# Optimization experiments

Measured on AMD Instinct MI355X. Metric: run time of the kernel, lower is better.

The kernel has to match this reference:

```python
import jax, jax.numpy as jnp
import numpy as np
from jax import lax

V = 5001   # vocab_size = len(word2id)+1
E = 128    # embedding_dim
H = 256    # hidden_dim
HH = H // 2  # per-direction hidden
T = 9      # tag_len
B, S = 256, 512


def setup_inputs() -> dict:
    key = jax.random.key(0)
    ks = jax.random.split(key, 16)
    sc = 0.08
    n = lambda k, shp: (jax.random.normal(k, shp) * sc).astype(jnp.float32)
    return {
        "x": jax.random.randint(ks[0], (B, S), 0, V),
        "mask": jnp.ones((B, S), jnp.float32),
        "embed_table": n(ks[1], (V, E)),
        "Wih_f": n(ks[2], (4 * HH, E)), "Whh_f": n(ks[3], (4 * HH, HH)),
        "bih_f": n(ks[4], (4 * HH,)), "bhh_f": n(ks[5], (4 * HH,)),
        "Wih_b": n(ks[6], (4 * HH, E)), "Whh_b": n(ks[7], (4 * HH, HH)),
        "bih_b": n(ks[8], (4 * HH,)), "bhh_b": n(ks[9], (4 * HH,)),
        "W_out": n(ks[10], (T, H)), "b_out": n(ks[11], (T,)),
        "transitions": n(ks[12], (T, T)),
        "start_trans": n(ks[13], (T,)),
        "end_trans": n(ks[14], (T,)),
    }


def _lstm_dir(xs, Wih, Whh, bih, bhh, reverse):
    # xs: [S,B,E]; torch gate order i,f,g,o
    Bx = xs.shape[1]
    h0 = jnp.zeros((Bx, HH), xs.dtype)
    pre_x = jnp.einsum('sbe,ge->sbg', xs, Wih) + bih + bhh  # hoist input proj

    def step(carry, px):
        h, c = carry
        g = px + h @ Whh.T
        i, f, gg, o = jnp.split(g, 4, axis=-1)
        c = jax.nn.sigmoid(f) * c + jax.nn.sigmoid(i) * jnp.tanh(gg)
        h = jax.nn.sigmoid(o) * jnp.tanh(c)
        return (h, c), h

    _, hs = lax.scan(step, (h0, h0), pre_x, reverse=reverse)
    return hs  # [S,B,HH]


def _viterbi(emissions, mask, transitions, start_trans, end_trans):
    # emissions: [B,S,T], mask: [B,S] bool -> tags [B,S] int32, best score [B]
    Bx = emissions.shape[0]
    em_t = emissions.transpose(1, 0, 2)        # [S,B,T]
    score0 = start_trans + em_t[0]             # [B,T]
    idT = jnp.arange(T, dtype=jnp.int32)

    def step(score, inp):
        em, m = inp                            # em [B,T], m [B]
        cand = score[:, :, None] + transitions[None]     # [B,Tprev,Tcur]
        best = jnp.max(cand, axis=1) + em
        bp = jnp.argmax(cand, axis=1).astype(jnp.int32)  # [B,T]
        new_score = jnp.where(m[:, None], best, score)
        bp = jnp.where(m[:, None], bp, idT[None, :])
        return new_score, bp

    score, bps = lax.scan(step, score0, (em_t[1:], mask.T[1:]))  # bps [S-1,B,T]
    score = score + end_trans
    best_score = jnp.max(score, axis=-1)                          # [B]
    last = jnp.argmax(score, axis=-1).astype(jnp.int32)           # [B]

    def back(tag, bp_t):
        prev = jnp.take_along_axis(bp_t, tag[:, None], axis=1)[:, 0]
        return prev, prev

    _, prevs = lax.scan(back, last, bps, reverse=True)            # [S-1,B]
    tags = jnp.concatenate([prevs, last[None, :]], axis=0).T      # [B,S]
    return tags, best_score


def reference(x, mask, embed_table, Wih_f, Whh_f, bih_f, bhh_f,
              Wih_b, Whh_b, bih_b, bhh_b, W_out, b_out,
              transitions, start_trans, end_trans):
    emb = embed_table[x]                       # [B,S,E]
    xs = emb.transpose(1, 0, 2)                # [S,B,E]
    hf = _lstm_dir(xs, Wih_f, Whh_f, bih_f, bhh_f, reverse=False)
    hb = _lstm_dir(xs, Wih_b, Whh_b, bih_b, bhh_b, reverse=True)
    hs = jnp.concatenate([hf, hb], axis=-1).transpose(1, 0, 2)   # [B,S,H]
    # dropout is identity at inference
    em = hs @ W_out.T + b_out                  # [B,S,T]
    em = em * mask[..., None]
    tags, best_score = _viterbi(em, mask > 0, transitions, start_trans, end_trans)
    return tags, best_score
```

## Files before the change

### kernel.cpp

```cpp
#include <hip/hip_runtime.h>
#include <hip/hip_bf16.h>
#include <math.h>

#define S_LEN 512
#define B_SZ  256
#define E_DIM 128
#define HHID  128
#define G4    512
#define T_TAG 9
#define NR    (S_LEN * B_SZ)
#define VOCAB 5001
#define VOCABP 5008

typedef __attribute__((ext_vector_type(8))) short bf16x8;
typedef __attribute__((ext_vector_type(4))) float f32x4;

__device__ __forceinline__ float bf2f(__hip_bfloat16 v) { return __bfloat162float(v); }
__device__ __forceinline__ float scrub0(float v) {
    unsigned u = __float_as_uint(v);
    return (((u >> 23) & 0xFFu) == 0xFFu) ? 0.f : v;
}
__device__ __forceinline__ float frcp(float x) { return __builtin_amdgcn_rcpf(x); }
__device__ __forceinline__ float fsig(float x) { return frcp(1.f + __expf(-x)); }
__device__ __forceinline__ float ftanh(float x) {
    return 1.f - 2.f * frcp(1.f + __expf(2.f * x));
}

__device__ __hip_bfloat16 g_emb[VOCAB * E_DIM];
__device__ __hip_bfloat16 g_wih[2][G4 * E_DIM];
__device__ __hip_bfloat16 g_whh2[2][G4 * HHID];
__device__ __align__(16) float g_bias[2][G4];
__device__ float g_wout[T_TAG * 256];
__device__ float g_bout[T_TAG];
__device__ float g_trans[T_TAG * T_TAG];
__device__ float g_start[T_TAG];
__device__ float g_end[T_TAG];
__device__ float g_maskf[B_SZ * S_LEN];
__device__ float g_em[(long)NR * T_TAG];
__device__ __align__(16) float g_hs[2][(long)NR * HHID];
__device__ __align__(16) float g_pxv[(long)2 * VOCABP * 128 * 4];

__global__ __launch_bounds__(256) void convert_kernel(
    const void* mask, const void* emb,
    const void* wih_f, const void* whh_f, const void* bih_f, const void* bhh_f,
    const void* wih_b, const void* whh_b, const void* bih_b, const void* bhh_b,
    const void* wout, const void* bout, const void* trans,
    const void* startt, const void* endt, float* out, int out_size)
{
    const bool isb = (((const unsigned*)mask)[0] == 0x3F803F80u);
    auto ldf = [&](const void* p, long i) -> float {
        float v = isb ? bf2f(((const __hip_bfloat16*)p)[i]) : ((const float*)p)[i];
        return scrub0(v);
    };
    const long tid0   = (long)blockIdx.x * blockDim.x + threadIdx.x;
    const long stride = (long)gridDim.x * blockDim.x;

    for (long i = tid0; i < out_size; i += stride) out[i] = 0.f;
    for (long i = tid0; i < (long)VOCAB * E_DIM; i += stride)
        g_emb[i] = __float2bfloat16(ldf(emb, i));
    for (long i = tid0; i < (long)G4 * E_DIM; i += stride) {
        const int np = (int)(i >> 7), e = (int)(i & 127);
        const int g = np & 3, u = np >> 2;
        const long src = (long)(g * 128 + u) * E_DIM + e;
        g_wih[0][i] = __float2bfloat16(ldf(wih_f, src));
        g_wih[1][i] = __float2bfloat16(ldf(wih_b, src));
    }
    for (long i = tid0; i < (long)G4 * HHID; i += stride) {
        const int np = (int)(i >> 7), k = (int)(i & 127);
        const int g = np & 3, u = np >> 2;
        const long src = (long)(g * 128 + u) * HHID + k;
        g_whh2[0][i] = __float2bfloat16(ldf(whh_f, src));
        g_whh2[1][i] = __float2bfloat16(ldf(whh_b, src));
    }
    for (long i = tid0; i < G4; i += stride) {
        const int g = (int)i & 3, u = (int)i >> 2;
        const long src = g * 128 + u;
        g_bias[0][i] = ldf(bih_f, src) + ldf(bhh_f, src);
        g_bias[1][i] = ldf(bih_b, src) + ldf(bhh_b, src);
    }
    for (long i = tid0; i < T_TAG * 256; i += stride) g_wout[i] = ldf(wout, i);
    for (long i = tid0; i < T_TAG * T_TAG; i += stride) g_trans[i] = ldf(trans, i);
    for (long i = tid0; i < T_TAG; i += stride) {
        g_bout[i]  = ldf(bout, i);
        g_start[i] = ldf(startt, i);
        g_end[i]   = ldf(endt, i);
    }
    for (long i = tid0; i < (long)B_SZ * S_LEN; i += stride)
        g_maskf[i] = ldf(mask, i);
}

__global__ __launch_bounds__(512, 2) void pxv_gemm()
{
    const int grp = blockIdx.x, dir = blockIdx.y;
    const int tid  = threadIdx.x;
    const int lane = tid & 63, wv = tid >> 6;
    const int m16  = lane & 15, quad = lane >> 4;

    bf16x8 V[4][4];
    f32x4 bias4[4];
    #pragma unroll
    for (int t = 0; t < 4; t++) {
        const int np = (wv * 4 + t) * 16 + m16;
        #pragma unroll
        for (int kk = 0; kk < 4; kk++)
            V[t][kk] = *(const bf16x8*)&g_wih[dir][(long)np * E_DIM + kk * 32 + quad * 8];
        const int u = 16 * wv + 4 * t + quad;
        const float4 b4 = *(const float4*)&g_bias[dir][4 * u];
        bias4[t] = (f32x4){b4.x, b4.y, b4.z, b4.w};
    }
    const int v  = grp * 16 + m16;
    const int vv = (v < VOCAB) ? v : 0;
    bf16x8 E[4];
    #pragma unroll
    for (int kk = 0; kk < 4; kk++)
        E[kk] = *(const bf16x8*)&g_emb[(long)vv * E_DIM + kk * 32 + quad * 8];
    #pragma unroll
    for (int t = 0; t < 4; t++) {
        f32x4 px = bias4[t];
        #pragma unroll
        for (int kk = 0; kk < 4; kk++)
            px = __builtin_amdgcn_mfma_f32_16x16x32_bf16(V[t][kk], E[kk], px, 0, 0, 0);
        const int u = 16 * wv + 4 * t + quad;
        if (v < VOCAB)
            *(f32x4*)&g_pxv[((long)(dir * VOCABP + v) * 128 + u) * 4] = px;
    }
}

#define SCAN_STEP(RD, PX)                                                      \
  {                                                                            \
    const int wr_ = (RD) ^ 1;                                                  \
        \
    int se2_ = sev + 2 * step;                                                 \
    se2_ = se2_ < 0 ? 0 : (se2_ > S_LEN - 1 ? S_LEN - 1 : se2_);               \
    const float* pf_ = pxvL + xO[se2_ * 16 + m16];                             \
    bf16x8 Hh_[4], Hl_[4];                                                     \
    _Pragma("unroll")                                                          \
    for (int kk = 0; kk < 4; kk++) {                                           \
        const int off_ = ((kk * 4 + quad) * 16 + m16) * 8;                     \
        Hh_[kk] = *(const bf16x8*)&hB[RD][0][off_];                            \
        Hl_[kk] = *(const bf16x8*)&hB[RD][1][off_];                            \
    }                                                                          \
    _Pragma("unroll")                                                          \
    for (int t = 0; t < 4; t++) {                                              \
        _Pragma("unroll")                                                      \
        for (int kk = 0; kk < 4; kk++) {                                       \
            PX[t] = __builtin_amdgcn_mfma_f32_16x16x32_bf16(W[t][kk], Hh_[kk], PX[t], 0, 0, 0); \
            PX[t] = __builtin_amdgcn_mfma_f32_16x16x32_bf16(W[t][kk], Hl_[kk], PX[t], 0, 0, 0); \
        }                                                                      \
    }                                                                          \
    _Pragma("unroll")                                                          \
    for (int t = 0; t < 4; t++) {                                              \
        const float iv = fsig(PX[t][0]);                                       \
        const float fv = fsig(PX[t][1]);                                       \
        const float gv = ftanh(PX[t][2]);                                      \
        const float ov = fsig(PX[t][3]);                                       \
        c[t] = fv * c[t] + iv * gv;                                            \
        const float h = ov * ftanh(c[t]);                                      \
        const int u = 16 * wv + 4 * t + quad;                                  \
        const unsigned ub = __float_as_uint(h);                                \
        const unsigned hb_ = ub >> 16;                                         \
        const float hif = __uint_as_float(ub & 0xFFFF0000u);                   \
        const unsigned lb_ = __float_as_uint(h - hif) >> 16;                   \
        const int ha = (u >> 3) * 128 + m16 * 8 + (u & 7);                     \
        hB[wr_][0][ha] = (unsigned short)hb_;                                  \
        hB[wr_][1][ha] = (unsigned short)lb_;                                  \
        hsp[t * 64] = h;                                                       \
    }                                                                          \
    {          \
        PX[0] = *(const f32x4*)(pf_ + 0);                                      \
        PX[1] = *(const f32x4*)(pf_ + 16);                                     \
        PX[2] = *(const f32x4*)(pf_ + 32);                                     \
        PX[3] = *(const f32x4*)(pf_ + 48);                                     \
    }                                                                          \
    asm volatile("s_waitcnt lgkmcnt(0)" ::: "memory");                         \
    __builtin_amdgcn_sched_barrier(0);                                         \
    __builtin_amdgcn_s_barrier();                                              \
    __builtin_amdgcn_sched_barrier(0);                                         \
    hsp += hsd; sev += step; itv++;                                            \
  }

__global__ __launch_bounds__(512, 2) void scan_mfma(const int* __restrict__ x)
{
    __shared__ __align__(16) unsigned short hB[2][2][16 * 16 * 8];
    __shared__ int xO[S_LEN * 16];

    const int bg = blockIdx.x, dir = blockIdx.y;
    const int tid  = threadIdx.x;
    const int lane = tid & 63, wv = tid >> 6;
    const int m16  = lane & 15, quad = lane >> 4;

    bf16x8 W[4][4];
    #pragma unroll
    for (int t = 0; t < 4; t++) {
        const int np = (wv * 4 + t) * 16 + m16;
        #pragma unroll
        for (int kk = 0; kk < 4; kk++)
            W[t][kk] = *(const bf16x8*)&g_whh2[dir][(long)np * HHID + kk * 32 + quad * 8];
    }
    {
        const bool x64 = ((x[1] | x[3] | x[5] | x[7]) == 0);
        for (int i = tid; i < S_LEN * 16; i += 512) {
            const int s = i >> 4, m = i & 15;
            const int ii = (bg * 16 + m) * S_LEN + s;
            int tok = x64 ? x[2 * ii] : x[ii];
            tok = (unsigned)tok < VOCAB ? tok : 0;
            xO[i] = tok * 512;
        }
    }
    for (int i = tid; i < 2 * 2 * 2048; i += 512) ((unsigned short*)hB)[i] = 0;
    float c[4] = {0.f, 0.f, 0.f, 0.f};
    __syncthreads();

    const int se0  = dir ? (S_LEN - 1) : 0;
    const int step = dir ? -1 : 1;
    const int u0   = 16 * wv + quad;

    const float* pxvL = &g_pxv[(long)dir * VOCABP * 512 + u0 * 4];

    f32x4 pxA[4], pxB[4];
    {
        const int o0 = xO[se0 * 16 + m16];
        #pragma unroll
        for (int t = 0; t < 4; t++) pxA[t] = *(const f32x4*)(pxvL + o0 + 16 * t);
        const int se1 = (S_LEN > 1) ? se0 + step : se0;
        const int o1 = xO[se1 * 16 + m16];
        #pragma unroll
        for (int t = 0; t < 4; t++) pxB[t] = *(const f32x4*)(pxvL + o1 + 16 * t);
    }

    float* hsp = &g_hs[dir][((long)(se0 * 16 + bg) * 128 + u0) * 16 + m16];
    const long hsd = (long)step * 32768;

    int itv = 0, sev = se0;

    for (int it = 0; it < S_LEN; it += 2) {
        SCAN_STEP(0, pxA)
        SCAN_STEP(1, pxB)
    }
}

__global__ __launch_bounds__(256, 4) void emission_kernel()
{
    __shared__ float hfL[2048], hbL[2048];
    __shared__ float Wsh[T_TAG][256];
    __shared__ float bo[T_TAG];
    const int tid = threadIdx.x, blk = blockIdx.x;
    for (int i = tid; i < T_TAG * 256; i += 256) Wsh[i >> 8][i & 255] = g_wout[i];
    if (tid < T_TAG) bo[tid] = g_bout[tid];
    const float* hf = &g_hs[0][(long)blk * 2048];
    const float* hb = &g_hs[1][(long)blk * 2048];
    for (int i = tid; i < 2048; i += 256) { hfL[i] = hf[i]; hbL[i] = hb[i]; }
    __syncthreads();

    const int m = tid & 15, j = tid >> 4;
    if (j < T_TAG) {
        float acc = bo[j];
        #pragma unroll 4
        for (int u = 0; u < 128; u++)
            acc += hfL[u * 16 + m] * Wsh[j][u] + hbL[u * 16 + m] * Wsh[j][128 + u];
        const int r = (blk >> 4) * 256 + (blk & 15) * 16 + m;
        g_em[(long)r * T_TAG + j] = scrub0(acc);
    }
}

__global__ __launch_bounds__(256, 2)
void viterbi_kernel(float* __restrict__ out, int out_size)
{
    __shared__ unsigned char bp[4][S_LEN][T_TAG];
    const int wid  = threadIdx.x >> 6;
    const int lane = threadIdx.x & 63;
    const int b  = blockIdx.x * 4 + wid;
    const int jj = (lane < T_TAG) ? lane : 0;

    float tcol[T_TAG];
    #pragma unroll
    for (int i = 0; i < T_TAG; i++) tcol[i] = g_trans[i * T_TAG + jj];

    float score[T_TAG];
    {
        const float m0 = g_maskf[b * S_LEN + 0];
        #pragma unroll
        for (int i = 0; i < T_TAG; i++)
            score[i] = g_start[i] + g_em[(long)b * T_TAG + i] * m0;
    }
    float e = g_em[((long)1 * B_SZ + b) * T_TAG + jj];
    float m = g_maskf[b * S_LEN + 1];

    for (int s = 1; s < S_LEN; s++) {
        float en = 0.f, mn = 0.f;
        if (s + 1 < S_LEN) {
            en = g_em[((long)(s + 1) * B_SZ + b) * T_TAG + jj];
            mn = g_maskf[b * S_LEN + s + 1];
        }
        float best = score[0] + tcol[0];
        int arg = 0;
        #pragma unroll
        for (int i = 1; i < T_TAG; i++) {
            const float cnd = score[i] + tcol[i];
            if (cnd > best) { best = cnd; arg = i; }
        }
        float ns; int nbp;
        if (m > 0.f) { ns = best + e * m; nbp = arg; }
        else         { ns = score[jj];    nbp = jj;  }
        if (lane < T_TAG) bp[wid][s][jj] = (unsigned char)nbp;
        #pragma unroll
        for (int i = 0; i < T_TAG; i++) score[i] = __shfl(ns, i, 64);
        e = en; m = mn;
    }
    #pragma unroll
    for (int i = 0; i < T_TAG; i++) score[i] += g_end[i];

    __syncthreads();

    if (lane == 0) {
        float bs = score[0]; int last = 0;
        #pragma unroll
        for (int i = 1; i < T_TAG; i++)
            if (score[i] > bs) { bs = score[i]; last = i; }
        {
            const unsigned u = __float_as_uint(bs);
            if (((u >> 23) & 0xFFu) == 0xFFu) bs = -100.f;
        }
        if ((long)B_SZ * S_LEN + b < out_size)
            out[(long)B_SZ * S_LEN + b] = bs;
        int tag = last;
        if (tag < 0) tag = 0; if (tag > 8) tag = 8;
        out[(long)b * S_LEN + (S_LEN - 1)] = (float)tag;
        for (int s2 = S_LEN - 1; s2 >= 1; s2--) {
            tag = bp[wid][s2][tag];
            if (tag < 0) tag = 0; if (tag > 8) tag = 8;
            out[(long)b * S_LEN + (s2 - 1)] = (float)tag;
        }
    }
}

extern "C" void kernel_launch(void* const* d_in, const int* in_sizes, int n_in,
                              void* d_out, int out_size, void* d_ws, size_t ws_size,
                              hipStream_t stream) {
    const int* x = (const int*)d_in[0];
    float* out = (float*)d_out;

    convert_kernel<<<512, 256, 0, stream>>>(
        d_in[1], d_in[2], d_in[3], d_in[4], d_in[5], d_in[6],
        d_in[7], d_in[8], d_in[9], d_in[10], d_in[11], d_in[12],
        d_in[13], d_in[14], d_in[15], out, out_size);
    pxv_gemm<<<dim3((VOCABP / 16), 2), 512, 0, stream>>>();
    scan_mfma<<<dim3(16, 2), 512, 0, stream>>>(x);
    emission_kernel<<<8192, 256, 0, stream>>>();
    viterbi_kernel<<<64, 256, 0, stream>>>(out, out_size);
}
```

Before: 928.7 us.

## Deepen scan input prefetch, vectorize embedding conversion, one-wave Viterbi blocks

```diff
diff --git a/kernel.cpp b/kernel.cpp
--- a/kernel.cpp
+++ b/kernel.cpp
@@ -14,6 +14,7 @@
 
 typedef __attribute__((ext_vector_type(8))) short bf16x8;
 typedef __attribute__((ext_vector_type(4))) float f32x4;
+typedef __attribute__((ext_vector_type(8))) unsigned short u16x8;
 
 __device__ __forceinline__ float bf2f(__hip_bfloat16 v) { return __bfloat162float(v); }
 __device__ __forceinline__ float scrub0(float v) {
@@ -56,8 +57,28 @@
     const long stride = (long)gridDim.x * blockDim.x;
 
     for (long i = tid0; i < out_size; i += stride) out[i] = 0.f;
-    for (long i = tid0; i < (long)VOCAB * E_DIM; i += stride)
-        g_emb[i] = __float2bfloat16(ldf(emb, i));
+
+    if (isb) {
+        const u16x8* src = (const u16x8*)emb;
+        u16x8* dst = (u16x8*)g_emb;
+        for (long i = tid0; i < (long)VOCAB * E_DIM / 8; i += stride) {
+            u16x8 v = src[i];
+            #pragma unroll
+            for (int j = 0; j < 8; j++)
+                if (((v[j] >> 7) & 0xFFu) == 0xFFu) v[j] = 0;
+            dst[i] = v;
+        }
+    } else {
+        const float4* src = (const float4*)emb;
+        for (long i = tid0; i < (long)VOCAB * E_DIM / 4; i += stride) {
+            const float4 v = src[i];
+            __hip_bfloat16* d = &g_emb[i * 4];
+            d[0] = __float2bfloat16(scrub0(v.x));
+            d[1] = __float2bfloat16(scrub0(v.y));
+            d[2] = __float2bfloat16(scrub0(v.z));
+            d[3] = __float2bfloat16(scrub0(v.w));
+        }
+    }
     for (long i = tid0; i < (long)G4 * E_DIM; i += stride) {
         const int np = (int)(i >> 7), e = (int)(i & 127);
         const int g = np & 3, u = np >> 2;
@@ -130,9 +151,9 @@
   {                                                                            \
     const int wr_ = (RD) ^ 1;                                                  \
         \
-    int se2_ = sev + 2 * step;                                                 \
-    se2_ = se2_ < 0 ? 0 : (se2_ > S_LEN - 1 ? S_LEN - 1 : se2_);               \
-    const float* pf_ = pxvL + xO[se2_ * 16 + m16];                             \
+    int se4_ = sev + 4 * step;                                                 \
+    se4_ = se4_ < 0 ? 0 : (se4_ > S_LEN - 1 ? S_LEN - 1 : se4_);               \
+    const float* pf_ = pxvL + xO[se4_ * 16 + m16];                             \
     bf16x8 Hh_[4], Hl_[4];                                                     \
     _Pragma("unroll")                                                          \
     for (int kk = 0; kk < 4; kk++) {                                           \
@@ -217,15 +238,19 @@
 
     const float* pxvL = &g_pxv[(long)dir * VOCABP * 512 + u0 * 4];
 
-    f32x4 pxA[4], pxB[4];
+    f32x4 pxA[4], pxB[4], pxC[4], pxD[4];
     {
-        const int o0 = xO[se0 * 16 + m16];
-        #pragma unroll
-        for (int t = 0; t < 4; t++) pxA[t] = *(const f32x4*)(pxvL + o0 + 16 * t);
-        const int se1 = (S_LEN > 1) ? se0 + step : se0;
-        const int o1 = xO[se1 * 16 + m16];
-        #pragma unroll
-        for (int t = 0; t < 4; t++) pxB[t] = *(const f32x4*)(pxvL + o1 + 16 * t);
+        const int o0 = xO[(se0)            * 16 + m16];
+        const int o1 = xO[(se0 + step)     * 16 + m16];
+        const int o2 = xO[(se0 + 2 * step) * 16 + m16];
+        const int o3 = xO[(se0 + 3 * step) * 16 + m16];
+        #pragma unroll
+        for (int t = 0; t < 4; t++) {
+            pxA[t] = *(const f32x4*)(pxvL + o0 + 16 * t);
+            pxB[t] = *(const f32x4*)(pxvL + o1 + 16 * t);
+            pxC[t] = *(const f32x4*)(pxvL + o2 + 16 * t);
+            pxD[t] = *(const f32x4*)(pxvL + o3 + 16 * t);
+        }
     }
 
     float* hsp = &g_hs[dir][((long)(se0 * 16 + bg) * 128 + u0) * 16 + m16];
@@ -233,9 +258,11 @@
 
     int itv = 0, sev = se0;
 
-    for (int it = 0; it < S_LEN; it += 2) {
+    for (int it = 0; it < S_LEN; it += 4) {
         SCAN_STEP(0, pxA)
         SCAN_STEP(1, pxB)
+        SCAN_STEP(0, pxC)
+        SCAN_STEP(1, pxD)
     }
 }
 
@@ -263,13 +290,12 @@
     }
 }
 
-__global__ __launch_bounds__(256, 2)
+__global__ __launch_bounds__(64, 1)
 void viterbi_kernel(float* __restrict__ out, int out_size)
 {
-    __shared__ unsigned char bp[4][S_LEN][T_TAG];
-    const int wid  = threadIdx.x >> 6;
-    const int lane = threadIdx.x & 63;
-    const int b  = blockIdx.x * 4 + wid;
+    __shared__ unsigned char bp[S_LEN][T_TAG];
+    const int lane = threadIdx.x;
+    const int b  = blockIdx.x;
     const int jj = (lane < T_TAG) ? lane : 0;
 
     float tcol[T_TAG];
@@ -302,7 +328,7 @@
         float ns; int nbp;
         if (m > 0.f) { ns = best + e * m; nbp = arg; }
         else         { ns = score[jj];    nbp = jj;  }
-        if (lane < T_TAG) bp[wid][s][jj] = (unsigned char)nbp;
+        if (lane < T_TAG) bp[s][jj] = (unsigned char)nbp;
         #pragma unroll
         for (int i = 0; i < T_TAG; i++) score[i] = __shfl(ns, i, 64);
         e = en; m = mn;
@@ -327,7 +353,7 @@
         if (tag < 0) tag = 0; if (tag > 8) tag = 8;
         out[(long)b * S_LEN + (S_LEN - 1)] = (float)tag;
         for (int s2 = S_LEN - 1; s2 >= 1; s2--) {
-            tag = bp[wid][s2][tag];
+            tag = bp[s2][tag];
             if (tag < 0) tag = 0; if (tag > 8) tag = 8;
             out[(long)b * S_LEN + (s2 - 1)] = (float)tag;
         }
@@ -347,5 +373,5 @@
     pxv_gemm<<<dim3((VOCABP / 16), 2), 512, 0, stream>>>();
     scan_mfma<<<dim3(16, 2), 512, 0, stream>>>(x);
     emission_kernel<<<8192, 256, 0, stream>>>();
-    viterbi_kernel<<<64, 256, 0, stream>>>(out, out_size);
-}
+    viterbi_kernel<<<256, 64, 0, stream>>>(out, out_size);
+}
```

After: 955.4 us. +2.9%, slower.
